# Kernel tuning notes

Measured on AMD Instinct MI355X. Metric: run time of the kernel, lower is better.

## Reference

```python
import jax, jax.numpy as jnp
import numpy as np

N_NODES = 50000
N_EDGES = 500000
D_MODEL = 128
NHEAD = 8
D_HEAD = 16
NUM_KEYS = 8
NUM_ETYPES = 4
NUM_STRINGS = 20000
NUM_BLOCKS = 2
N_TARGETS = 128


def setup_inputs() -> dict:
    key = jax.random.key(0)
    ks = jax.random.split(key, 16)
    s = 1.0 / np.sqrt(D_MODEL)
    return {
        "emb": jax.random.normal(ks[0], (NUM_STRINGS, D_MODEL), jnp.float32) * s,
        "query_w": jax.random.normal(ks[1], (NUM_BLOCKS, NUM_KEYS, NHEAD, D_HEAD, D_MODEL), jnp.float32) * s,
        "key_w": jax.random.normal(ks[2], (NUM_BLOCKS, NUM_ETYPES, NHEAD, D_HEAD, D_MODEL), jnp.float32) * s,
        "value_w": jax.random.normal(ks[3], (NUM_BLOCKS, NUM_ETYPES, NHEAD, D_HEAD, D_MODEL), jnp.float32) * s,
        "node_w": jax.random.normal(ks[4], (NUM_BLOCKS, NUM_KEYS, NHEAD, D_HEAD, D_MODEL), jnp.float32) * s,
        "target_w": jax.random.normal(ks[5], (NUM_BLOCKS, NUM_KEYS, NHEAD, D_HEAD), jnp.float32) * s,
        "ln_gamma": jnp.ones((NUM_BLOCKS, D_MODEL), jnp.float32),
        "ln_beta": jnp.zeros((NUM_BLOCKS, D_MODEL), jnp.float32),
        "value_ids": jax.random.randint(ks[6], (N_NODES,), 0, NUM_STRINGS),
        "key_ids": jax.random.randint(ks[7], (N_NODES,), 0, NUM_KEYS),
        "src": jax.random.randint(ks[8], (N_EDGES,), 0, N_NODES),
        "dst": jax.random.randint(ks[9], (N_EDGES,), 0, N_NODES),
        "etype": jax.random.randint(ks[10], (N_EDGES,), 0, NUM_ETYPES),
        "target_idx": jax.random.randint(ks[11], (N_TARGETS,), 0, N_NODES),
    }


def _layer_norm(x, g, b, eps=1e-5):
    mu = jnp.mean(x, -1, keepdims=True)
    var = jnp.var(x, -1, keepdims=True)
    return (x - mu) * jax.lax.rsqrt(var + eps) * g + b


def _per_type_proj(feat, w, type_ids):
    # feat: [N,D], w: [T,H,Dh,D] -> project for all types then select the
    # node's/edge-endpoint's own type (identical math to gathering w[type]).
    all_t = jnp.einsum("nd,thfd->nthf", feat, w)  # [N,T,H,Dh]
    return jnp.take_along_axis(all_t, type_ids[:, None, None, None], axis=1)[:, 0]


def _hetero_attn_conv(feat, qw, kw, vw, nw, lg, lb, key_ids, src, dst, etype):
    n = feat.shape[0]
    q = _per_type_proj(feat, qw, key_ids)                     # [N,H,Dh] per-key query
    k_all = jnp.einsum("nd,thfd->nthf", feat, kw)             # [N,T,H,Dh]
    v_all = jnp.einsum("nd,thfd->nthf", feat, vw)
    k_e = k_all[src, etype]                                   # [E,H,Dh] per-etype key
    v_e = v_all[src, etype]                                   # [E,H,Dh]
    scale = np.float32(1.0 / np.sqrt(D_HEAD))
    scores = jnp.sum(q[dst] * k_e, -1) * scale                # [E,H]
    # edge softmax over incoming edges of each dst node
    m = jax.ops.segment_max(scores, dst, num_segments=n)      # [N,H]
    e = jnp.exp(scores - m[dst])
    z = jax.ops.segment_sum(e, dst, num_segments=n)
    attn = e / (z[dst] + 1e-9)                                # [E,H]
    agg = jax.ops.segment_sum(attn[..., None] * v_e, dst, num_segments=n)
    agg = agg.reshape(n, D_MODEL)
    h = _per_type_proj(agg, nw, key_ids).reshape(n, D_MODEL)  # per-key node proj
    h = jax.nn.relu(h)                                        # node_activation='relu'
    return _layer_norm(h, lg, lb)                             # norm=True


def reference(emb, query_w, key_w, value_w, node_w, target_w, ln_gamma, ln_beta,
              value_ids, key_ids, src, dst, etype, target_idx):
    feat = emb[value_ids]  # ValueEmbedding lookup [N,D]
    target_keys = key_ids[target_idx]
    outs = []
    for i in range(NUM_BLOCKS):
        prev = feat
        feat = _hetero_attn_conv(feat, query_w[i], key_w[i], value_w[i], node_w[i],
                                 ln_gamma[i], ln_beta[i], key_ids, src, dst, etype)
        feat = feat + prev  # block_residual=True (conv_residual=False)
        tf = feat[target_idx].reshape(N_TARGETS, NHEAD, D_HEAD)
        tw = target_w[i][target_keys]  # [B,H,Dh]
        outs.append(jnp.sum(tf * tw, axis=(1, 2)))  # Target readout per block
    out = jnp.mean(jnp.stack(outs, -1), -1)  # mean over block outputs
    return out  # [N_TARGETS] (single target)
```

## Files before the change

### kernel.cpp

```cpp
#include <hip/hip_runtime.h>
#include <hip/hip_bf16.h>

#define N_NODES   50000
#define N_EDGES   500000
#define NHEAD     8
#define NUM_KEYS  8
#define NUM_ETYPES 4
#define NUM_BLOCKS 2
#define N_TARGETS 128
#define NPAD      51200
#define NTILES    400
#define NBLK      196
#define LDW       136
#define LDWF      132
#define QKVW      1152
#define SCAP      45

typedef unsigned short u16;
typedef unsigned int   u32;
typedef __attribute__((ext_vector_type(8))) short short8;
typedef __attribute__((ext_vector_type(4))) short short4v;
typedef __attribute__((ext_vector_type(4))) float floatx4;

__device__ __forceinline__ size_t pkaddr(int tile, int r, int c){
  return (size_t)tile * 16384 + ((c >> 3) << 10) + (r << 3) + (c & 7);
}

__device__ __forceinline__ float bflo(u32 u)  { return __uint_as_float(u << 16); }
__device__ __forceinline__ float bfhi(u32 u)  { return __uint_as_float(u & 0xffff0000u); }
__device__ __forceinline__ float bf2f(u16 u)  { return __uint_as_float(((u32)u) << 16); }
__device__ __forceinline__ u16   f2bf(float f){
  u32 u = __float_as_uint(f);
  u += 0x7fffu + ((u >> 16) & 1u);
  return (u16)(u >> 16);
}

__global__ void detect_dtype(const u16* raw, int* flag){
  __shared__ int cnt;
  if (threadIdx.x == 0) cnt = 0;
  __syncthreads();
  int sane = 0;
  #pragma unroll
  for (int k = 0; k < 4; k++){
    u16 u = raw[threadIdx.x * 4 + k];
    int e = (u >> 7) & 0xff;
    if (e >= 100 && e <= 145) sane++;
  }
  atomicAdd(&cnt, sane);
  __syncthreads();
  if (threadIdx.x == 0) *flag = (cnt >= 870) ? 1 : 0;
}

__global__ void cvt_f32(const void* src, float* dst, int n, const int* flag){
  int i = blockIdx.x * 256 + threadIdx.x;
  if (i >= n) return;
  dst[i] = (*flag) ? bf2f(((const u16*)src)[i]) : ((const float*)src)[i];
}
__global__ void cvt_packw(const void* src, size_t soff, u16* dst, int n, const int* flag){
  int i = blockIdx.x * 256 + threadIdx.x;
  if (i >= n) return;
  u16 v = (*flag) ? ((const u16*)src)[soff + i] : f2bf(((const float*)src)[soff + i]);
  int mat = i >> 14, rem = i & 16383;
  int row = rem >> 7, k = rem & 127;
  dst[pkaddr(mat, row, k)] = v;
}

__global__ void khist_blk(const int* __restrict__ key_ids, int* __restrict__ blkcnt){
  __shared__ int c[8];
  int t = threadIdx.x, b = blockIdx.x;
  if (t < 8) c[t] = 0;
  __syncthreads();
  int n = b * 256 + t;
  if (n < N_NODES) atomicAdd(&c[key_ids[n]], 1);
  __syncthreads();
  if (t < 8) blkcnt[t * NBLK + b] = c[t];
}
__global__ void kscan2(const int* __restrict__ blkcnt, int* __restrict__ base,
                       int* __restrict__ tile_key){
  __shared__ int po[8];
  __shared__ int tot[8];
  int t = threadIdx.x;
  if (t < 8){
    int s = 0;
    for (int b = 0; b < NBLK; b++) s += blkcnt[t * NBLK + b];
    tot[t] = s;
  }
  __syncthreads();
  if (t == 0){
    int off = 0;
    for (int k = 0; k < 8; k++){ po[k] = off; off += ((tot[k] + 127) >> 7) << 7; }
  }
  __syncthreads();
  if (t < 8){
    int run = po[t];
    for (int b = 0; b < NBLK; b++){ base[t * NBLK + b] = run; run += blkcnt[t * NBLK + b]; }
  }
  for (int tt = t; tt < NTILES; tt += 64){
    int row = tt << 7, k = 7;
    for (int kk = 1; kk < 8; kk++)
      if (row < po[kk]){ k = kk - 1; break; }
    tile_key[tt] = k;
  }
}
__global__ void scatter_perm2(const int* __restrict__ key_ids, const int* __restrict__ base,
                              int* __restrict__ perm, int* __restrict__ invperm){
  __shared__ unsigned char keyarr[256];
  int t = threadIdx.x, b = blockIdx.x;
  int n = b * 256 + t;
  int key = (n < N_NODES) ? key_ids[n] : 8;
  keyarr[t] = (unsigned char)key;
  __syncthreads();
  if (n >= N_NODES) return;
  int rank = 0;
  for (int j = 0; j < t; j++) rank += (keyarr[j] == (unsigned char)key);
  int pos = base[key * NBLK + b] + rank;
  perm[pos] = n;
  invperm[n] = pos;
}

__global__ void gather_feat(const void* emb_raw, const int* __restrict__ vid,
                            const int* __restrict__ perm, const int* __restrict__ flag,
                            float* __restrict__ feat, u16* __restrict__ fhi,
                            u16* __restrict__ flo){
  int i = blockIdx.x * 256 + threadIdx.x;
  int n = i >> 7, d = i & 127;
  int e = (vid[perm[n]] << 7) + d;
  float v = (*flag) ? bf2f(((const u16*)emb_raw)[e]) : ((const float*)emb_raw)[e];
  feat[i] = v;
  u16 h = f2bf(v);
  size_t pa = pkaddr(n >> 7, n & 127, d);
  fhi[pa] = h;
  flo[pa] = f2bf(v - bf2f(h));
}

__global__ void hist_dst(const int* __restrict__ dst, const int* __restrict__ invp,
                         int* __restrict__ deg){
  int e = blockIdx.x * 256 + threadIdx.x;
  if (e < N_EDGES) atomicAdd(&deg[invp[dst[e]]], 1);
}
__global__ __launch_bounds__(1024) void scan_deg(const int* __restrict__ deg,
                                                 int* __restrict__ rs, int* __restrict__ cur){
  __shared__ int s[1024];
  int t = threadIdx.x;
  int lo = t * 50, hi = lo + 50;
  int sum = 0;
  for (int i = lo; i < hi; i++) sum += deg[i];
  s[t] = sum;
  __syncthreads();
  for (int off = 1; off < 1024; off <<= 1){
    int v = (t >= off) ? s[t - off] : 0;
    __syncthreads();
    s[t] += v;
    __syncthreads();
  }
  int run = s[t] - sum;
  for (int i = lo; i < hi; i++){
    rs[i] = run; cur[i] = run;
    run += deg[i];
  }
}
__global__ void scatter_edges(const int* __restrict__ src, const int* __restrict__ dst,
                              const int* __restrict__ et, const int* __restrict__ invp,
                              int* __restrict__ cur, u32* __restrict__ epk){
  int e = blockIdx.x * 256 + threadIdx.x;
  if (e >= N_EDGES) return;
  int pos = atomicAdd(&cur[invp[dst[e]]], 1);
  epk[pos] = ((u32)invp[src[e]] << 2) | (u32)et[e];
}
__global__ __launch_bounds__(256) void sort_csr(const int* __restrict__ rs,
                                                const int* __restrict__ deg,
                                                u32* __restrict__ epk){
  __shared__ u32 buf[256 * SCAP];
  int t = threadIdx.x;
  int n = blockIdx.x * 256 + t;
  if (n >= NPAD) return;
  int s = rs[n], c = deg[n];
  if (c <= 1) return;
  if (c <= SCAP){
    u32* b = buf + t * SCAP;
    for (int i = 0; i < c; i++) b[i] = epk[s + i];
    for (int i = 1; i < c; i++){
      u32 v = b[i];
      int j = i - 1;
      while (j >= 0 && b[j] > v){ b[j + 1] = b[j]; j--; }
      b[j + 1] = v;
    }
    for (int i = 0; i < c; i++) epk[s + i] = b[i];
  } else {
    for (int i = 1; i < c; i++){
      u32 v = epk[s + i];
      int j = i - 1;
      while (j >= 0 && epk[s + j] > v){ epk[s + j + 1] = epk[s + j]; j--; }
      epk[s + j + 1] = v;
    }
  }
}

__global__ __launch_bounds__(256) void gemm_qkv(
    const u16* __restrict__ Ahi, const u16* __restrict__ Alo,
    const u16* __restrict__ Qw, const u16* __restrict__ KVw,
    const int* __restrict__ tkey, u16* __restrict__ C)
{
  __shared__ u16 sc[128 * LDW];
  int id = blockIdx.x;
  int xcd = id & 7, wi = id >> 3;
  int cy = xcd * 50 + wi / 9;
  int cx = wi % 9;
  int m0 = cy * 128;
  const u16* Bte = (cx == 0) ? (Qw + (size_t)tkey[cy] * 16384)
                             : (KVw + (size_t)(cx - 1) * 16384);
  const u16* Ath = Ahi + (size_t)cy * 16384;
  const u16* Atl = Alo + (size_t)cy * 16384;
  int w = threadIdx.x >> 6, l = threadIdx.x & 63;
  int wm = (w & 1) * 64, wn = (w >> 1) * 64;
  int lr = l & 15, lg = l >> 4;
  floatx4 acc[4][4] = {};
  #pragma unroll
  for (int kk = 0; kk < 4; kk++){
    int cc10 = (kk * 4 + lg) << 10;
    short8 ah[4], al[4], bfr[4];
    #pragma unroll
    for (int i = 0; i < 4; i++){
      int off = cc10 + ((wm + i * 16 + lr) << 3);
      ah[i] = *(const short8*)(Ath + off);
      al[i] = *(const short8*)(Atl + off);
    }
    #pragma unroll
    for (int j = 0; j < 4; j++)
      bfr[j] = *(const short8*)(Bte + cc10 + ((wn + j * 16 + lr) << 3));
    #pragma unroll
    for (int i = 0; i < 4; i++)
      #pragma unroll
      for (int j = 0; j < 4; j++){
        acc[i][j] = __builtin_amdgcn_mfma_f32_16x16x32_bf16(ah[i], bfr[j], acc[i][j], 0, 0, 0);
        acc[i][j] = __builtin_amdgcn_mfma_f32_16x16x32_bf16(al[i], bfr[j], acc[i][j], 0, 0, 0);
      }
  }
  #pragma unroll
  for (int i = 0; i < 4; i++)
    #pragma unroll
    for (int j = 0; j < 4; j++)
      #pragma unroll
      for (int r = 0; r < 4; r++)
        sc[(wm + i * 16 + lg * 4 + r) * LDW + wn + j * 16 + lr] = f2bf(acc[i][j][r]);
  __syncthreads();
  int tr = threadIdx.x >> 4, tc = (threadIdx.x & 15) * 8;
  int cbase = cx * 128;
  #pragma unroll
  for (int it = 0; it < 8; it++){
    int row = tr + it * 16;
    short8 vv = *(const short8*)(sc + row * LDW + tc);
    *(short8*)(C + (size_t)(m0 + row) * QKVW + cbase + tc) = vv;
  }
}

__global__ __launch_bounds__(256) void gemm_h_ln(
    const u16* __restrict__ Ahi, const u16* __restrict__ Alo,
    const u16* __restrict__ Bt, const int* __restrict__ tkey,
    const float* __restrict__ gbf,
    float* __restrict__ feat, u16* __restrict__ fhi, u16* __restrict__ flo, int blk)
{
  __shared__ float scf[64 * LDWF];
  int m0 = blockIdx.x * 64;
  int tile = blockIdx.x >> 1, rbase = (blockIdx.x & 1) * 64;
  const u16* Bte = Bt + (size_t)tkey[tile] * 16384;
  const u16* Ath = Ahi + (size_t)tile * 16384;
  const u16* Atl = Alo + (size_t)tile * 16384;
  int w = threadIdx.x >> 6, l = threadIdx.x & 63;
  int wn = w * 32;
  int lr = l & 15, lg = l >> 4;
  floatx4 acc[4][2] = {};
  #pragma unroll
  for (int kk = 0; kk < 4; kk++){
    int cc10 = (kk * 4 + lg) << 10;
    short8 ah[4], al[4], bfr[2];
    #pragma unroll
    for (int i = 0; i < 4; i++){
      int off = cc10 + ((rbase + i * 16 + lr) << 3);
      ah[i] = *(const short8*)(Ath + off);
      al[i] = *(const short8*)(Atl + off);
    }
    #pragma unroll
    for (int j = 0; j < 2; j++)
      bfr[j] = *(const short8*)(Bte + cc10 + ((wn + j * 16 + lr) << 3));
    #pragma unroll
    for (int i = 0; i < 4; i++)
      #pragma unroll
      for (int j = 0; j < 2; j++){
        acc[i][j] = __builtin_amdgcn_mfma_f32_16x16x32_bf16(ah[i], bfr[j], acc[i][j], 0, 0, 0);
        acc[i][j] = __builtin_amdgcn_mfma_f32_16x16x32_bf16(al[i], bfr[j], acc[i][j], 0, 0, 0);
      }
  }
  #pragma unroll
  for (int i = 0; i < 4; i++)
    #pragma unroll
    for (int j = 0; j < 2; j++)
      #pragma unroll
      for (int r = 0; r < 4; r++)
        scf[(i * 16 + lg * 4 + r) * LDWF + wn + j * 16 + lr] = acc[i][j][r];
  __syncthreads();
  int r = threadIdx.x >> 2, q4 = (threadIdx.x & 3) * 32;
  const float* srow = scf + r * LDWF + q4;
  float s1 = 0.f, s2 = 0.f;
  #pragma unroll
  for (int c = 0; c < 32; c++){
    float v = fmaxf(srow[c], 0.f);
    s1 += v; s2 += v * v;
  }
  s1 += __shfl_xor(s1, 1, 64); s1 += __shfl_xor(s1, 2, 64);
  s2 += __shfl_xor(s2, 1, 64); s2 += __shfl_xor(s2, 2, 64);
  float mu = s1 * (1.f / 128.f);
  float var = s2 * (1.f / 128.f) - mu * mu;
  float rstd = rsqrtf(var + 1e-5f);
  int n = m0 + r;
  int ntile = n >> 7, nr = n & 127;
  float* fr = feat + (size_t)n * 128 + q4;
  const float* gp = gbf + (blk << 7) + q4;
  #pragma unroll
  for (int c = 0; c < 32; c += 4){
    float4 fo = *(float4*)(fr + c);
    float y0 = (fmaxf(srow[c+0], 0.f) - mu) * rstd * gp[c+0] + gp[256 + c + 0] + fo.x;
    float y1 = (fmaxf(srow[c+1], 0.f) - mu) * rstd * gp[c+1] + gp[256 + c + 1] + fo.y;
    float y2 = (fmaxf(srow[c+2], 0.f) - mu) * rstd * gp[c+2] + gp[256 + c + 2] + fo.z;
    float y3 = (fmaxf(srow[c+3], 0.f) - mu) * rstd * gp[c+3] + gp[256 + c + 3] + fo.w;
    *(float4*)(fr + c) = make_float4(y0, y1, y2, y3);
    u16 h0 = f2bf(y0), h1 = f2bf(y1), h2 = f2bf(y2), h3 = f2bf(y3);
    size_t pa = pkaddr(ntile, nr, q4 + c);
    short4v ph; ph.x = (short)h0; ph.y = (short)h1; ph.z = (short)h2; ph.w = (short)h3;
    *(short4v*)(fhi + pa) = ph;
    short4v pl;
    pl.x = (short)f2bf(y0 - bf2f(h0)); pl.y = (short)f2bf(y1 - bf2f(h1));
    pl.z = (short)f2bf(y2 - bf2f(h2)); pl.w = (short)f2bf(y3 - bf2f(h3));
    *(short4v*)(flo + pa) = pl;
  }
}

__device__ __forceinline__ float dot8(uint4 a, uint4 b){
  return bflo(a.x)*bflo(b.x) + bfhi(a.x)*bfhi(b.x)
       + bflo(a.y)*bflo(b.y) + bfhi(a.y)*bfhi(b.y)
       + bflo(a.z)*bflo(b.z) + bfhi(a.z)*bfhi(b.z)
       + bflo(a.w)*bflo(b.w) + bfhi(a.w)*bfhi(b.w);
}

__global__ __launch_bounds__(256) void edge_attn(
    const u16* __restrict__ qkv,
    const int* __restrict__ rs, const int* __restrict__ deg,
    const u32* __restrict__ epk, u16* __restrict__ agghi, u16* __restrict__ agglo)
{
  int n = blockIdx.x * 4 + (threadIdx.x >> 6);
  int l = threadIdx.x & 63;
  int h = l & 7, s = l >> 3;
  const u16* qp = qkv + (size_t)n * QKVW + (h << 4);
  uint4 q0 = *(const uint4*)qp, q1 = *(const uint4*)(qp + 8);
  int e0 = rs[n], cnt = deg[n];
  float z = 0.f;
  float acc[16];
  #pragma unroll
  for (int j = 0; j < 16; j++) acc[j] = 0.f;
  for (int base = 0; base < cnt; base += 16){
    int idx0 = base + s, idx1 = base + s + 8;
    bool p0 = idx0 < cnt, p1 = idx1 < cnt;
    u32 pk0 = p0 ? epk[e0 + idx0] : 0u;
    u32 pk1 = p1 ? epk[e0 + idx1] : 0u;
    const u16* kp0 = qkv + (size_t)(pk0 >> 2) * QKVW + 128 + ((pk0 & 3) << 7) + (h << 4);
    const u16* kp1 = qkv + (size_t)(pk1 >> 2) * QKVW + 128 + ((pk1 & 3) << 7) + (h << 4);
    if (p0){
      uint4 k0 = *(const uint4*)kp0, k1 = *(const uint4*)(kp0 + 8);
      float sc = (dot8(q0, k0) + dot8(q1, k1)) * 0.25f;
      float ew = __expf(fminf(sc, 80.f));
      const u16* vp = kp0 + 512;
      uint4 v0 = *(const uint4*)vp, v1 = *(const uint4*)(vp + 8);
      z += ew;
      acc[0]  += ew * bflo(v0.x); acc[1]  += ew * bfhi(v0.x);
      acc[2]  += ew * bflo(v0.y); acc[3]  += ew * bfhi(v0.y);
      acc[4]  += ew * bflo(v0.z); acc[5]  += ew * bfhi(v0.z);
      acc[6]  += ew * bflo(v0.w); acc[7]  += ew * bfhi(v0.w);
      acc[8]  += ew * bflo(v1.x); acc[9]  += ew * bfhi(v1.x);
      acc[10] += ew * bflo(v1.y); acc[11] += ew * bfhi(v1.y);
      acc[12] += ew * bflo(v1.z); acc[13] += ew * bfhi(v1.z);
      acc[14] += ew * bflo(v1.w); acc[15] += ew * bfhi(v1.w);
    }
    if (p1){
      uint4 k0 = *(const uint4*)kp1, k1 = *(const uint4*)(kp1 + 8);
      float sc = (dot8(q0, k0) + dot8(q1, k1)) * 0.25f;
      float ew = __expf(fminf(sc, 80.f));
      const u16* vp = kp1 + 512;
      uint4 v0 = *(const uint4*)vp, v1 = *(const uint4*)(vp + 8);
      z += ew;
      acc[0]  += ew * bflo(v0.x); acc[1]  += ew * bfhi(v0.x);
      acc[2]  += ew * bflo(v0.y); acc[3]  += ew * bfhi(v0.y);
      acc[4]  += ew * bflo(v0.z); acc[5]  += ew * bfhi(v0.z);
      acc[6]  += ew * bflo(v0.w); acc[7]  += ew * bfhi(v0.w);
      acc[8]  += ew * bflo(v1.x); acc[9]  += ew * bfhi(v1.x);
      acc[10] += ew * bflo(v1.y); acc[11] += ew * bfhi(v1.y);
      acc[12] += ew * bflo(v1.z); acc[13] += ew * bfhi(v1.z);
      acc[14] += ew * bflo(v1.w); acc[15] += ew * bfhi(v1.w);
    }
  }
  #pragma unroll
  for (int m = 8; m < 64; m <<= 1){
    z += __shfl_xor(z, m, 64);
    #pragma unroll
    for (int j = 0; j < 16; j++) acc[j] += __shfl_xor(acc[j], m, 64);
  }
  float inv = 1.f / (z + 1e-9f);
  int j0 = s * 2;
  float x0 = acc[j0] * inv, x1 = acc[j0 + 1] * inv;
  u16 h0 = f2bf(x0), h1 = f2bf(x1);
  int col = (h << 4) + j0;
  size_t pa = pkaddr(n >> 7, n & 127, col);
  *(u32*)(agghi + pa) = (u32)h0 | ((u32)h1 << 16);
  *(u32*)(agglo + pa) = (u32)f2bf(x0 - bf2f(h0)) | ((u32)f2bf(x1 - bf2f(h1)) << 16);
}

__global__ __launch_bounds__(128) void readout(
    const float* __restrict__ feat, const float* __restrict__ twf,
    const int* __restrict__ key_ids, const int* __restrict__ invp,
    const int* __restrict__ tgt,
    float* __restrict__ outacc, void* dout, const int* __restrict__ flag, int blk)
{
  int t = threadIdx.x;
  int n = tgt[t];
  int key = key_ids[n];
  const float* fr = feat + (size_t)invp[n] * 128;
  const float* wr = twf + (size_t)((blk * 8 + key) << 7);
  float acc = 0.f;
  #pragma unroll
  for (int d = 0; d < 128; d++) acc = fmaf(fr[d], wr[d], acc);
  if (blk == 0){
    outacc[t] = 0.5f * acc;
  } else {
    float r = outacc[t] + 0.5f * acc;
    if (*flag) ((u16*)dout)[t] = f2bf(r);
    else       ((float*)dout)[t] = r;
  }
}

extern "C" void kernel_launch(void* const* d_in, const int* in_sizes, int n_in,
                              void* d_out, int out_size, void* d_ws, size_t ws_size,
                              hipStream_t stream)
{
  const void* emb = d_in[0];
  const void* qw  = d_in[1];
  const void* kw  = d_in[2];
  const void* vw  = d_in[3];
  const void* nw  = d_in[4];
  const void* tw  = d_in[5];
  const void* lg  = d_in[6];
  const void* lb  = d_in[7];
  const int* value_ids = (const int*)d_in[8];
  const int* key_ids   = (const int*)d_in[9];
  const int* srcp  = (const int*)d_in[10];
  const int* dstp  = (const int*)d_in[11];
  const int* etp   = (const int*)d_in[12];
  const int* tgt   = (const int*)d_in[13];

  char* p = (char*)d_ws;
  auto carve = [&](size_t bytes)->char*{
    char* r = p; p += (bytes + 255) & ~(size_t)255; return r;
  };
  int*   flag    = (int*)  carve(4);
  float* featp   = (float*)carve((size_t)NPAD * 128 * 4);
  u16*   feathi  = (u16*)  carve((size_t)NPAD * 128 * 2);
  u16*   featlo  = (u16*)  carve((size_t)NPAD * 128 * 2);
  u16*   qwc     = (u16*)  carve((size_t)2 * 1024 * 128 * 2);
  u16*   kvw     = (u16*)  carve((size_t)2 * 1024 * 128 * 2);
  u16*   nwc     = (u16*)  carve((size_t)2 * 1024 * 128 * 2);
  float* twf     = (float*)carve((size_t)2048 * 4);
  float* gbf     = (float*)carve((size_t)512 * 4);
  int*   blkcnt  = (int*)  carve((size_t)8 * NBLK * 4);
  int*   kbase   = (int*)  carve((size_t)8 * NBLK * 4);
  int*   tile_key= (int*)  carve(NTILES * 4);
  int*   perm    = (int*)  carve((size_t)NPAD * 4);
  int*   invperm = (int*)  carve((size_t)N_NODES * 4);
  int*   deg     = (int*)  carve((size_t)NPAD * 4);
  int*   rsx     = (int*)  carve((size_t)NPAD * 4);
  int*   cur     = (int*)  carve((size_t)NPAD * 4);
  u32*   epk     = (u32*)  carve((size_t)N_EDGES * 4);
  u16*   qkvbuf  = (u16*)  carve((size_t)NPAD * QKVW * 2);
  u16*   agghi   = (u16*)  carve((size_t)NPAD * 128 * 2);
  u16*   agglo   = (u16*)  carve((size_t)NPAD * 128 * 2);
  float* outacc  = (float*)carve((size_t)N_TARGETS * 4);
  (void)ws_size; (void)n_in; (void)in_sizes; (void)out_size;

  detect_dtype<<<1, 256, 0, stream>>>((const u16*)emb, flag);

  auto cpk = [&](const void* s, size_t so, u16* d, int n){
    cvt_packw<<<(n + 255) / 256, 256, 0, stream>>>(s, so, d, n, flag);
  };
  cpk(qw, 0, qwc, 2 * 1024 * 128);
  cpk(nw, 0, nwc, 2 * 1024 * 128);
  for (int b = 0; b < 2; b++){
    cpk(kw, (size_t)b * 512 * 128, kvw + (size_t)b * 1024 * 128,             512 * 128);
    cpk(vw, (size_t)b * 512 * 128, kvw + (size_t)b * 1024 * 128 + 512 * 128, 512 * 128);
  }
  cvt_f32<<<8, 256, 0, stream>>>(tw, twf, 2048, flag);
  cvt_f32<<<1, 256, 0, stream>>>(lg, gbf, 256, flag);
  cvt_f32<<<1, 256, 0, stream>>>(lb, gbf + 256, 256, flag);

  hipMemsetAsync(perm, 0, (size_t)NPAD * 4, stream);
  khist_blk<<<NBLK, 256, 0, stream>>>(key_ids, blkcnt);
  kscan2<<<1, 64, 0, stream>>>(blkcnt, kbase, tile_key);
  scatter_perm2<<<NBLK, 256, 0, stream>>>(key_ids, kbase, perm, invperm);

  gather_feat<<<(NPAD * 128) / 256, 256, 0, stream>>>(emb, value_ids, perm, flag,
                                                      featp, feathi, featlo);

  hipMemsetAsync(deg, 0, (size_t)NPAD * 4, stream);
  const int eg = (N_EDGES + 255) / 256;
  hist_dst<<<eg, 256, 0, stream>>>(dstp, invperm, deg);
  scan_deg<<<1, 1024, 0, stream>>>(deg, rsx, cur);
  scatter_edges<<<eg, 256, 0, stream>>>(srcp, dstp, etp, invperm, cur, epk);
  sort_csr<<<(NPAD + 255) / 256, 256, 0, stream>>>(rsx, deg, epk);

  for (int b = 0; b < NUM_BLOCKS; b++){
    gemm_qkv<<<3600, 256, 0, stream>>>(feathi, featlo,
                                       qwc + (size_t)b * 1024 * 128,
                                       kvw + (size_t)b * 1024 * 128,
                                       tile_key, qkvbuf);
    edge_attn<<<NPAD / 4, 256, 0, stream>>>(qkvbuf, rsx, deg, epk, agghi, agglo);
    gemm_h_ln<<<NPAD / 64, 256, 0, stream>>>(agghi, agglo,
                                             nwc + (size_t)b * 1024 * 128,
                                             tile_key, gbf, featp, feathi, featlo, b);
    readout<<<1, 128, 0, stream>>>(featp, twf, key_ids, invperm, tgt, outacc, d_out, flag, b);
  }
}
```

Baseline: 503.1 us.

## Remap edge attention to 16 lanes per node and fuse setup conversion kernels

Edge attention now gives each node 16 lanes instead of a 64-lane wavefront. It processes 4 edges per iteration with packed float2 math, clamped (always-valid) loads and a single cross-lane shuffle step, and writes 8 outputs per lane as vector stores. This targets the idle lanes and long shuffle reduction of the old mapping at an average degree of about 10 edges. The separate weight and parameter conversion launches are merged into one kernel, the degree memset is folded into gather_feat, and the readout dot product is vectorized with float4 loads. In exchange, nodes with high degree get less parallelism per node, and edges past the end redo a load of the last valid edge.

```diff
diff --git a/kernel.cpp b/kernel.cpp
--- a/kernel.cpp
+++ b/kernel.cpp
@@ -21,6 +21,7 @@
 typedef __attribute__((ext_vector_type(8))) short short8;
 typedef __attribute__((ext_vector_type(4))) short short4v;
 typedef __attribute__((ext_vector_type(4))) float floatx4;
+typedef __attribute__((ext_vector_type(2))) float f32x2;
 
 __device__ __forceinline__ size_t pkaddr(int tile, int r, int c){
   return (size_t)tile * 16384 + ((c >> 3) << 10) + (r << 3) + (c & 7);
@@ -34,6 +35,9 @@
   u += 0x7fffu + ((u >> 16) & 1u);
   return (u16)(u >> 16);
 }
+__device__ __forceinline__ f32x2 up2(u32 u){
+  f32x2 r; r.x = bflo(u); r.y = bfhi(u); return r;
+}
 
 __global__ void detect_dtype(const u16* raw, int* flag){
   __shared__ int cnt;
@@ -51,18 +55,37 @@
   if (threadIdx.x == 0) *flag = (cnt >= 870) ? 1 : 0;
 }
 
-__global__ void cvt_f32(const void* src, float* dst, int n, const int* flag){
-  int i = blockIdx.x * 256 + threadIdx.x;
-  if (i >= n) return;
-  dst[i] = (*flag) ? bf2f(((const u16*)src)[i]) : ((const float*)src)[i];
-}
-__global__ void cvt_packw(const void* src, size_t soff, u16* dst, int n, const int* flag){
-  int i = blockIdx.x * 256 + threadIdx.x;
-  if (i >= n) return;
-  u16 v = (*flag) ? ((const u16*)src)[soff + i] : f2bf(((const float*)src)[soff + i]);
-  int mat = i >> 14, rem = i & 16383;
-  int row = rem >> 7, k = rem & 127;
-  dst[pkaddr(mat, row, k)] = v;
+__global__ void cvt_all(const void* qw, const void* nw, const void* kw, const void* vw,
+                        const void* tw, const void* lgp, const void* lbp,
+                        u16* __restrict__ qwc, u16* __restrict__ nwc, u16* __restrict__ kvw,
+                        float* __restrict__ twf, float* __restrict__ gbf,
+                        const int* __restrict__ flag){
+  int b = blockIdx.x, t = threadIdx.x;
+  int fl = *flag;
+  if (b < 2048){
+    const void* src = (b < 1024) ? qw : nw;
+    u16* dst = (b < 1024) ? qwc : nwc;
+    int i = ((b & 1023) << 8) + t;
+    u16 v = fl ? ((const u16*)src)[i] : f2bf(((const float*)src)[i]);
+    int mat = i >> 14, rem = i & 16383;
+    dst[pkaddr(mat, rem >> 7, rem & 127)] = v;
+  } else if (b < 3072){
+    int r = b - 2048;
+    int blk = r >> 9, half = (r >> 8) & 1;
+    int i = ((r & 255) << 8) + t;
+    const void* src = half ? vw : kw;
+    size_t soff = (size_t)blk * 65536 + i;
+    u16 v = fl ? ((const u16*)src)[soff] : f2bf(((const float*)src)[soff]);
+    int mat = i >> 14, rem = i & 16383;
+    kvw[(size_t)blk * 131072 + (size_t)half * 65536 + pkaddr(mat, rem >> 7, rem & 127)] = v;
+  } else if (b < 3080){
+    int i = ((b - 3072) << 8) + t;
+    twf[i] = fl ? bf2f(((const u16*)tw)[i]) : ((const float*)tw)[i];
+  } else if (b == 3080){
+    gbf[t] = fl ? bf2f(((const u16*)lgp)[t]) : ((const float*)lgp)[t];
+  } else {
+    gbf[256 + t] = fl ? bf2f(((const u16*)lbp)[t]) : ((const float*)lbp)[t];
+  }
 }
 
 __global__ void khist_blk(const int* __restrict__ key_ids, int* __restrict__ blkcnt){
@@ -121,9 +144,10 @@
 __global__ void gather_feat(const void* emb_raw, const int* __restrict__ vid,
                             const int* __restrict__ perm, const int* __restrict__ flag,
                             float* __restrict__ feat, u16* __restrict__ fhi,
-                            u16* __restrict__ flo){
+                            u16* __restrict__ flo, int* __restrict__ deg){
   int i = blockIdx.x * 256 + threadIdx.x;
   int n = i >> 7, d = i & 127;
+  if (d == 0) deg[n] = 0;
   int e = (vid[perm[n]] << 7) + d;
   float v = (*flag) ? bf2f(((const u16*)emb_raw)[e]) : ((const float*)emb_raw)[e];
   feat[i] = v;
@@ -335,82 +359,79 @@
   }
 }
 
-__device__ __forceinline__ float dot8(uint4 a, uint4 b){
-  return bflo(a.x)*bflo(b.x) + bfhi(a.x)*bfhi(b.x)
-       + bflo(a.y)*bflo(b.y) + bfhi(a.y)*bfhi(b.y)
-       + bflo(a.z)*bflo(b.z) + bfhi(a.z)*bfhi(b.z)
-       + bflo(a.w)*bflo(b.w) + bfhi(a.w)*bfhi(b.w);
-}
-
 __global__ __launch_bounds__(256) void edge_attn(
     const u16* __restrict__ qkv,
     const int* __restrict__ rs, const int* __restrict__ deg,
     const u32* __restrict__ epk, u16* __restrict__ agghi, u16* __restrict__ agglo)
 {
-  int n = blockIdx.x * 4 + (threadIdx.x >> 6);
-  int l = threadIdx.x & 63;
+  int n = blockIdx.x * 16 + (threadIdx.x >> 4);
+  int l = threadIdx.x & 15;
   int h = l & 7, s = l >> 3;
   const u16* qp = qkv + (size_t)n * QKVW + (h << 4);
   uint4 q0 = *(const uint4*)qp, q1 = *(const uint4*)(qp + 8);
+  f32x2 qv[8];
+  qv[0] = up2(q0.x); qv[1] = up2(q0.y); qv[2] = up2(q0.z); qv[3] = up2(q0.w);
+  qv[4] = up2(q1.x); qv[5] = up2(q1.y); qv[6] = up2(q1.z); qv[7] = up2(q1.w);
   int e0 = rs[n], cnt = deg[n];
   float z = 0.f;
-  float acc[16];
-  #pragma unroll
-  for (int j = 0; j < 16; j++) acc[j] = 0.f;
-  for (int base = 0; base < cnt; base += 16){
-    int idx0 = base + s, idx1 = base + s + 8;
-    bool p0 = idx0 < cnt, p1 = idx1 < cnt;
-    u32 pk0 = p0 ? epk[e0 + idx0] : 0u;
-    u32 pk1 = p1 ? epk[e0 + idx1] : 0u;
+  f32x2 acc[8];
+  #pragma unroll
+  for (int j = 0; j < 8; j++){ acc[j].x = 0.f; acc[j].y = 0.f; }
+  for (int base = 0; base < cnt; base += 4){
+    int i0 = base + s, i1 = base + s + 2;
+    bool p0 = i0 < cnt, p1 = i1 < cnt;
+    u32 pk0 = epk[e0 + min(i0, cnt - 1)];
+    u32 pk1 = epk[e0 + min(i1, cnt - 1)];
     const u16* kp0 = qkv + (size_t)(pk0 >> 2) * QKVW + 128 + ((pk0 & 3) << 7) + (h << 4);
     const u16* kp1 = qkv + (size_t)(pk1 >> 2) * QKVW + 128 + ((pk1 & 3) << 7) + (h << 4);
-    if (p0){
-      uint4 k0 = *(const uint4*)kp0, k1 = *(const uint4*)(kp0 + 8);
-      float sc = (dot8(q0, k0) + dot8(q1, k1)) * 0.25f;
-      float ew = __expf(fminf(sc, 80.f));
-      const u16* vp = kp0 + 512;
-      uint4 v0 = *(const uint4*)vp, v1 = *(const uint4*)(vp + 8);
-      z += ew;
-      acc[0]  += ew * bflo(v0.x); acc[1]  += ew * bfhi(v0.x);
-      acc[2]  += ew * bflo(v0.y); acc[3]  += ew * bfhi(v0.y);
-      acc[4]  += ew * bflo(v0.z); acc[5]  += ew * bfhi(v0.z);
-      acc[6]  += ew * bflo(v0.w); acc[7]  += ew * bfhi(v0.w);
-      acc[8]  += ew * bflo(v1.x); acc[9]  += ew * bfhi(v1.x);
-      acc[10] += ew * bflo(v1.y); acc[11] += ew * bfhi(v1.y);
-      acc[12] += ew * bflo(v1.z); acc[13] += ew * bfhi(v1.z);
-      acc[14] += ew * bflo(v1.w); acc[15] += ew * bfhi(v1.w);
-    }
-    if (p1){
-      uint4 k0 = *(const uint4*)kp1, k1 = *(const uint4*)(kp1 + 8);
-      float sc = (dot8(q0, k0) + dot8(q1, k1)) * 0.25f;
-      float ew = __expf(fminf(sc, 80.f));
-      const u16* vp = kp1 + 512;
-      uint4 v0 = *(const uint4*)vp, v1 = *(const uint4*)(vp + 8);
-      z += ew;
-      acc[0]  += ew * bflo(v0.x); acc[1]  += ew * bfhi(v0.x);
-      acc[2]  += ew * bflo(v0.y); acc[3]  += ew * bfhi(v0.y);
-      acc[4]  += ew * bflo(v0.z); acc[5]  += ew * bfhi(v0.z);
-      acc[6]  += ew * bflo(v0.w); acc[7]  += ew * bfhi(v0.w);
-      acc[8]  += ew * bflo(v1.x); acc[9]  += ew * bfhi(v1.x);
-      acc[10] += ew * bflo(v1.y); acc[11] += ew * bfhi(v1.y);
-      acc[12] += ew * bflo(v1.z); acc[13] += ew * bfhi(v1.z);
-      acc[14] += ew * bflo(v1.w); acc[15] += ew * bfhi(v1.w);
-    }
-  }
-  #pragma unroll
-  for (int m = 8; m < 64; m <<= 1){
-    z += __shfl_xor(z, m, 64);
-    #pragma unroll
-    for (int j = 0; j < 16; j++) acc[j] += __shfl_xor(acc[j], m, 64);
+    uint4 ka0 = *(const uint4*)kp0, kb0 = *(const uint4*)(kp0 + 8);
+    uint4 va0 = *(const uint4*)(kp0 + 512), vb0 = *(const uint4*)(kp0 + 520);
+    uint4 ka1 = *(const uint4*)kp1, kb1 = *(const uint4*)(kp1 + 8);
+    uint4 va1 = *(const uint4*)(kp1 + 512), vb1 = *(const uint4*)(kp1 + 520);
+    f32x2 d0 = up2(ka0.x) * qv[0] + up2(ka0.y) * qv[1] + up2(ka0.z) * qv[2] + up2(ka0.w) * qv[3]
+             + up2(kb0.x) * qv[4] + up2(kb0.y) * qv[5] + up2(kb0.z) * qv[6] + up2(kb0.w) * qv[7];
+    f32x2 d1 = up2(ka1.x) * qv[0] + up2(ka1.y) * qv[1] + up2(ka1.z) * qv[2] + up2(ka1.w) * qv[3]
+             + up2(kb1.x) * qv[4] + up2(kb1.y) * qv[5] + up2(kb1.z) * qv[6] + up2(kb1.w) * qv[7];
+    float ew0 = p0 ? __expf(fminf((d0.x + d0.y) * 0.25f, 80.f)) : 0.f;
+    float ew1 = p1 ? __expf(fminf((d1.x + d1.y) * 0.25f, 80.f)) : 0.f;
+    z += ew0 + ew1;
+    f32x2 w0v; w0v.x = ew0; w0v.y = ew0;
+    f32x2 w1v; w1v.x = ew1; w1v.y = ew1;
+    acc[0] += w0v * up2(va0.x); acc[1] += w0v * up2(va0.y);
+    acc[2] += w0v * up2(va0.z); acc[3] += w0v * up2(va0.w);
+    acc[4] += w0v * up2(vb0.x); acc[5] += w0v * up2(vb0.y);
+    acc[6] += w0v * up2(vb0.z); acc[7] += w0v * up2(vb0.w);
+    acc[0] += w1v * up2(va1.x); acc[1] += w1v * up2(va1.y);
+    acc[2] += w1v * up2(va1.z); acc[3] += w1v * up2(va1.w);
+    acc[4] += w1v * up2(vb1.x); acc[5] += w1v * up2(vb1.y);
+    acc[6] += w1v * up2(vb1.z); acc[7] += w1v * up2(vb1.w);
+  }
+  z += __shfl_xor(z, 8, 64);
+  #pragma unroll
+  for (int j = 0; j < 8; j++){
+    acc[j].x += __shfl_xor(acc[j].x, 8, 64);
+    acc[j].y += __shfl_xor(acc[j].y, 8, 64);
   }
   float inv = 1.f / (z + 1e-9f);
-  int j0 = s * 2;
-  float x0 = acc[j0] * inv, x1 = acc[j0 + 1] * inv;
-  u16 h0 = f2bf(x0), h1 = f2bf(x1);
-  int col = (h << 4) + j0;
-  size_t pa = pkaddr(n >> 7, n & 127, col);
-  *(u32*)(agghi + pa) = (u32)h0 | ((u32)h1 << 16);
-  *(u32*)(agglo + pa) = (u32)f2bf(x0 - bf2f(h0)) | ((u32)f2bf(x1 - bf2f(h1)) << 16);
+  float xv[8];
+  if (s == 0){
+    xv[0] = acc[0].x; xv[1] = acc[0].y; xv[2] = acc[1].x; xv[3] = acc[1].y;
+    xv[4] = acc[2].x; xv[5] = acc[2].y; xv[6] = acc[3].x; xv[7] = acc[3].y;
+  } else {
+    xv[0] = acc[4].x; xv[1] = acc[4].y; xv[2] = acc[5].x; xv[3] = acc[5].y;
+    xv[4] = acc[6].x; xv[5] = acc[6].y; xv[6] = acc[7].x; xv[7] = acc[7].y;
+  }
+  short8 ph, pl;
+  #pragma unroll
+  for (int k = 0; k < 8; k++){
+    float y = xv[k] * inv;
+    u16 hk = f2bf(y);
+    ph[k] = (short)hk;
+    pl[k] = (short)f2bf(y - bf2f(hk));
+  }
+  size_t pa = pkaddr(n >> 7, n & 127, (h << 4) + (s << 3));
+  *(short8*)(agghi + pa) = ph;
+  *(short8*)(agglo + pa) = pl;
 }
 
 __global__ __launch_bounds__(128) void readout(
@@ -422,11 +443,14 @@
   int t = threadIdx.x;
   int n = tgt[t];
   int key = key_ids[n];
-  const float* fr = feat + (size_t)invp[n] * 128;
-  const float* wr = twf + (size_t)((blk * 8 + key) << 7);
+  const float4* fr = (const float4*)(feat + (size_t)invp[n] * 128);
+  const float4* wr = (const float4*)(twf + (size_t)((blk * 8 + key) << 7));
   float acc = 0.f;
   #pragma unroll
-  for (int d = 0; d < 128; d++) acc = fmaf(fr[d], wr[d], acc);
+  for (int d = 0; d < 32; d++){
+    float4 a = fr[d], b = wr[d];
+    acc += a.x * b.x + a.y * b.y + a.z * b.z + a.w * b.w;
+  }
   if (blk == 0){
     outacc[t] = 0.5f * acc;
   } else {
@@ -485,18 +509,8 @@
 
   detect_dtype<<<1, 256, 0, stream>>>((const u16*)emb, flag);
 
-  auto cpk = [&](const void* s, size_t so, u16* d, int n){
-    cvt_packw<<<(n + 255) / 256, 256, 0, stream>>>(s, so, d, n, flag);
-  };
-  cpk(qw, 0, qwc, 2 * 1024 * 128);
-  cpk(nw, 0, nwc, 2 * 1024 * 128);
-  for (int b = 0; b < 2; b++){
-    cpk(kw, (size_t)b * 512 * 128, kvw + (size_t)b * 1024 * 128,             512 * 128);
-    cpk(vw, (size_t)b * 512 * 128, kvw + (size_t)b * 1024 * 128 + 512 * 128, 512 * 128);
-  }
-  cvt_f32<<<8, 256, 0, stream>>>(tw, twf, 2048, flag);
-  cvt_f32<<<1, 256, 0, stream>>>(lg, gbf, 256, flag);
-  cvt_f32<<<1, 256, 0, stream>>>(lb, gbf + 256, 256, flag);
+  cvt_all<<<3082, 256, 0, stream>>>(qw, nw, kw, vw, tw, lg, lb,
+                                    qwc, nwc, kvw, twf, gbf, flag);
 
   hipMemsetAsync(perm, 0, (size_t)NPAD * 4, stream);
   khist_blk<<<NBLK, 256, 0, stream>>>(key_ids, blkcnt);
@@ -504,9 +518,8 @@
   scatter_perm2<<<NBLK, 256, 0, stream>>>(key_ids, kbase, perm, invperm);
 
   gather_feat<<<(NPAD * 128) / 256, 256, 0, stream>>>(emb, value_ids, perm, flag,
-                                                      featp, feathi, featlo);
-
-  hipMemsetAsync(deg, 0, (size_t)NPAD * 4, stream);
+                                                      featp, feathi, featlo, deg);
+
   const int eg = (N_EDGES + 255) / 256;
   hist_dst<<<eg, 256, 0, stream>>>(dstp, invperm, deg);
   scan_deg<<<1, 1024, 0, stream>>>(deg, rsx, cur);
@@ -518,7 +531,7 @@
                                        qwc + (size_t)b * 1024 * 128,
                                        kvw + (size_t)b * 1024 * 128,
                                        tile_key, qkvbuf);
-    edge_attn<<<NPAD / 4, 256, 0, stream>>>(qkvbuf, rsx, deg, epk, agghi, agglo);
+    edge_attn<<<NPAD / 16, 256, 0, stream>>>(qkvbuf, rsx, deg, epk, agghi, agglo);
     gemm_h_ln<<<NPAD / 64, 256, 0, stream>>>(agghi, agglo,
                                              nwc + (size_t)b * 1024 * 128,
                                              tile_key, gbf, featp, feathi, featlo, b);
```

Measured after the change: 484.8 us. -3.6%, faster.
